# Kernel optimization log

Measured on AMD Instinct MI355X. Metric: run time of the kernel, lower is better.

## Reference

```python
import jax, jax.numpy as jnp
import numpy as np


def _grid_sample_paste(m, boxes, img_h, img_w):
    """Bilinear, align_corners=False, zero padding; separable because the
    affine grid is an outer product of per-row and per-col coordinates.
    m: [N, Hm, Wm] float, boxes: [N, 4] xyxy in output-image coords.
    Returns [N, img_h, img_w]."""
    N, Hm, Wm = m.shape
    x0, y0, x1, y1 = boxes[:, 0:1], boxes[:, 1:2], boxes[:, 2:3], boxes[:, 3:4]
    ys = jnp.arange(img_h, dtype=m.dtype) + 0.5  # pixel centers
    xs = jnp.arange(img_w, dtype=m.dtype) + 0.5
    gy = (ys[None, :] - y0) / (y1 - y0) * 2 - 1  # [N, img_h] in [-1,1]
    gx = (xs[None, :] - x0) / (x1 - x0) * 2 - 1  # [N, img_w]
    # align_corners=False: pixel coord = (g+1)*size/2 - 0.5
    py = (gy + 1) * (Hm * 0.5) - 0.5
    px = (gx + 1) * (Wm * 0.5) - 0.5

    def interp(vals, p, axis, size):
        f = jnp.floor(p)
        i0 = f.astype(jnp.int32)
        w1 = (p - f).astype(vals.dtype)
        w0 = 1.0 - w1

        def gather(idx):
            valid = ((idx >= 0) & (idx < size)).astype(vals.dtype)
            idxc = jnp.clip(idx, 0, size - 1)
            if axis == 2:
                g = jnp.take_along_axis(vals, idxc[:, None, :], axis=2)
                return g * valid[:, None, :]
            else:
                g = jnp.take_along_axis(vals, idxc[:, :, None], axis=1)
                return g * valid[:, :, None]

        if axis == 2:
            return gather(i0) * w0[:, None, :] + gather(i0 + 1) * w1[:, None, :]
        else:
            return gather(i0) * w0[:, :, None] + gather(i0 + 1) * w1[:, :, None]

    mx = interp(m, px, axis=2, size=Wm)   # [N, Hm, img_w]
    return interp(mx, py, axis=1, size=Hm)  # [N, img_h, img_w]


def setup_inputs() -> dict:
    key = jax.random.key(0)
    k1, k2, k3, k4, k5 = jax.random.split(key, 5)
    N, Hm, Wm = 128, 28, 28
    in_h, in_w = 736, 1184
    img_h, img_w = 800, 1280
    masks = jax.random.uniform(k1, (N, 1, Hm, Wm), dtype=jnp.float32)
    # valid xyxy boxes in detector-input coordinates
    bx0 = jax.random.uniform(k2, (N,), minval=0.0, maxval=in_w - 64.0)
    by0 = jax.random.uniform(k3, (N,), minval=0.0, maxval=in_h - 64.0)
    bw = 16.0 + jax.random.uniform(k4, (N,), maxval=256.0)
    bh = 16.0 + jax.random.uniform(k5, (N,), maxval=256.0)
    boxes = jnp.stack([bx0, by0,
                       jnp.minimum(bx0 + bw, in_w * 1.0),
                       jnp.minimum(by0 + bh, in_h * 1.0)], axis=1).astype(jnp.float32)
    return {"masks": masks, "boxes": boxes, "img_h": img_h, "img_w": img_w,
            "in_h": in_h, "in_w": in_w}


def reference(masks, boxes, img_h, img_w, in_h, in_w):
    # my_detector_postprocess: scale boxes to output resolution, clip to image
    sx = img_w / in_w
    sy = img_h / in_h
    scale = jnp.array([sx, sy, sx, sy], dtype=boxes.dtype)
    b = boxes * scale
    b = jnp.stack([jnp.clip(b[:, 0], 0.0, img_w), jnp.clip(b[:, 1], 0.0, img_h),
                   jnp.clip(b[:, 2], 0.0, img_w), jnp.clip(b[:, 3], 0.0, img_h)], axis=1)
    # my_paste_masks_in_image (GPU path, skip_empty=False), soft masks returned
    return _grid_sample_paste(masks[:, 0], b, img_h, img_w)
```

## Files before the change

kernel.cpp:

```cpp
#include <hip/hip_runtime.h>
#include <math.h>

__global__ __launch_bounds__(256) void zero_out(float4* __restrict__ out4, int nf4,
                                                float* __restrict__ out, int out_size) {
    int gid = blockIdx.x * blockDim.x + threadIdx.x;
    int stride = gridDim.x * blockDim.x;
    const float4 z = make_float4(0.f, 0.f, 0.f, 0.f);
    for (int i = gid; i < nf4; i += stride) out4[i] = z;
    if (gid == 0) {
        for (int k = nf4 * 4; k < out_size; ++k) out[k] = 0.f;
    }
}

__device__ __forceinline__ float bilin(const float* __restrict__ r0,
                                       const float* __restrict__ r1,
                                       float px, float vy0, float vy1, int Wm) {
    float fx = floorf(px);
    int ix = (int)fx;
    float wx1 = px - fx;
    float wx0 = 1.f - wx1;
    float vx0 = (ix >= 0 && ix < Wm) ? wx0 : 0.f;
    float vx1 = (ix + 1 >= 0 && ix + 1 < Wm) ? wx1 : 0.f;
    int rx0 = min(max(ix, 0), Wm - 1);
    int rx1 = min(max(ix + 1, 0), Wm - 1);
    float top = r0[rx0] * vx0 + r0[rx1] * vx1;
    float bot = r1[rx0] * vx0 + r1[rx1] * vx1;
    return top * vy0 + bot * vy1;
}

__global__ __launch_bounds__(128) void paint_box(const float* __restrict__ masks,
                       const float* __restrict__ boxes,
                       const int* __restrict__ p_img_h,
                       const int* __restrict__ p_img_w,
                       const int* __restrict__ p_in_h,
                       const int* __restrict__ p_in_w,
                       float* __restrict__ out,
                       int HW, int Hm, int Wm) {
    const int n = blockIdx.x;
    const int img_w = p_img_w[0];
    const int img_h = HW / img_w;

    float fw = (float)img_w, fh = (float)img_h;
    float sx = fw / (float)p_in_w[0];
    float sy = fh / (float)p_in_h[0];
    float x0 = fminf(fmaxf(boxes[4*n+0] * sx, 0.f), fw);
    float y0 = fminf(fmaxf(boxes[4*n+1] * sy, 0.f), fh);
    float x1 = fminf(fmaxf(boxes[4*n+2] * sx, 0.f), fw);
    float y1 = fminf(fmaxf(boxes[4*n+3] * sy, 0.f), fh);
    float swx = (float)Wm / (x1 - x0);
    float swy = (float)Hm / (y1 - y0);

    int xlo = max(0,     (int)floorf(x0 - 0.5f / swx - 0.5f) - 1);
    int xhi = min(img_w, (int)ceilf (x0 + ((float)Wm + 0.5f) / swx - 0.5f) + 2);
    int ylo = max(0,     (int)floorf(y0 - 0.5f / swy - 0.5f) - 1);
    int yhi = min(img_h, (int)ceilf (y0 + ((float)Hm + 0.5f) / swy - 0.5f) + 2);

    const float* mb = masks + (size_t)n * Hm * Wm;
    float* ob = out + (size_t)n * HW;

    for (int y = ylo + blockIdx.y; y < yhi; y += gridDim.y) {
        float py = ((float)y + 0.5f - y0) * swy - 0.5f;
        float fy = floorf(py);
        int iy = (int)fy;
        float wy1 = py - fy, wy0 = 1.f - wy1;
        float vy0 = (iy >= 0 && iy < Hm) ? wy0 : 0.f;
        float vy1 = (iy + 1 >= 0 && iy + 1 < Hm) ? wy1 : 0.f;
        const float* r0 = mb + (size_t)min(max(iy, 0), Hm - 1) * Wm;
        const float* r1 = mb + (size_t)min(max(iy + 1, 0), Hm - 1) * Wm;
        float* orow = ob + (size_t)y * img_w;
        for (int x = xlo + (int)threadIdx.x; x < xhi; x += (int)blockDim.x) {
            float px = ((float)x + 0.5f - x0) * swx - 0.5f;
            orow[x] = bilin(r0, r1, px, vy0, vy1, Wm);
        }
    }
}

extern "C" void kernel_launch(void* const* d_in, const int* in_sizes, int n_in,
                              void* d_out, int out_size, void* d_ws, size_t ws_size,
                              hipStream_t stream) {
    const float* masks  = (const float*)d_in[0];
    const float* boxes  = (const float*)d_in[1];
    const int* p_img_h  = (const int*)d_in[2];
    const int* p_img_w  = (const int*)d_in[3];
    const int* p_in_h   = (const int*)d_in[4];
    const int* p_in_w   = (const int*)d_in[5];

    int N = in_sizes[1] / 4;
    int mask_hw = in_sizes[0] / N;
    int Wm = (int)(sqrtf((float)mask_hw) + 0.5f);
    int Hm = mask_hw / Wm;
    int HW = out_size / N;

    int nf4 = out_size / 4;
    int zblocks = 4096;
    hipLaunchKernelGGL(zero_out, dim3(zblocks), dim3(256), 0, stream,
                       (float4*)d_out, nf4, (float*)d_out, out_size);

    hipLaunchKernelGGL(paint_box, dim3(N, 512), dim3(128), 0, stream,
                       masks, boxes, p_img_h, p_img_w, p_in_h, p_in_w,
                       (float*)d_out, HW, Hm, Wm);
}
```

Measured before the change: 553.9 us.

## Fuse zero-fill and box painting into a single full-image row kernel

Drops the separate zero-fill pass. A new single kernel writes every output pixel once: one block per image row per mask, and each thread produces a float4 of four pixels, storing zeros outside the box. Per-box parameters are precomputed by a tiny setup kernel into workspace. This removes the double write to the box region and the poor occupancy of the old per-box loop, at the cost of an extra small launch and a generic slow fallback path for other image widths.

New measurement: 523.8 us. 5.4% less time.

```diff
diff --git a/kernel.cpp b/kernel.cpp
--- a/kernel.cpp
+++ b/kernel.cpp
@@ -1,20 +1,28 @@
 #include <hip/hip_runtime.h>
 #include <math.h>
 
-__global__ __launch_bounds__(256) void zero_out(float4* __restrict__ out4, int nf4,
-                                                float* __restrict__ out, int out_size) {
-    int gid = blockIdx.x * blockDim.x + threadIdx.x;
-    int stride = gridDim.x * blockDim.x;
-    const float4 z = make_float4(0.f, 0.f, 0.f, 0.f);
-    for (int i = gid; i < nf4; i += stride) out4[i] = z;
-    if (gid == 0) {
-        for (int k = nf4 * 4; k < out_size; ++k) out[k] = 0.f;
-    }
+#define ROWTPB 320
+
+__global__ __launch_bounds__(128) void setup_params(
+        const float* __restrict__ boxes,
+        const int* __restrict__ p_img_h, const int* __restrict__ p_img_w,
+        const int* __restrict__ p_in_h,  const int* __restrict__ p_in_w,
+        float4* __restrict__ params, int N, int Hm, int Wm) {
+    int n = blockIdx.x * blockDim.x + threadIdx.x;
+    if (n >= N) return;
+    float fw = (float)p_img_w[0], fh = (float)p_img_h[0];
+    float sx = fw / (float)p_in_w[0];
+    float sy = fh / (float)p_in_h[0];
+    float x0 = fminf(fmaxf(boxes[4*n+0] * sx, 0.f), fw);
+    float y0 = fminf(fmaxf(boxes[4*n+1] * sy, 0.f), fh);
+    float x1 = fminf(fmaxf(boxes[4*n+2] * sx, 0.f), fw);
+    float y1 = fminf(fmaxf(boxes[4*n+3] * sy, 0.f), fh);
+    params[n] = make_float4(x0, y0, (float)Wm / (x1 - x0), (float)Hm / (y1 - y0));
 }
 
-__device__ __forceinline__ float bilin(const float* __restrict__ r0,
-                                       const float* __restrict__ r1,
-                                       float px, float vy0, float vy1, int Wm) {
+__device__ __forceinline__ float bilinx(const float* __restrict__ r0,
+                                        const float* __restrict__ r1,
+                                        float px, float vy0, float vy1, int Wm) {
     float fx = floorf(px);
     int ix = (int)fx;
     float wx1 = px - fx;
@@ -23,54 +31,77 @@
     float vx1 = (ix + 1 >= 0 && ix + 1 < Wm) ? wx1 : 0.f;
     int rx0 = min(max(ix, 0), Wm - 1);
     int rx1 = min(max(ix + 1, 0), Wm - 1);
-    float top = r0[rx0] * vx0 + r0[rx1] * vx1;
-    float bot = r1[rx0] * vx0 + r1[rx1] * vx1;
-    return top * vy0 + bot * vy1;
+    return (r0[rx0] * vx0 + r0[rx1] * vx1) * vy0
+         + (r1[rx0] * vx0 + r1[rx1] * vx1) * vy1;
 }
 
-__global__ __launch_bounds__(128) void paint_box(const float* __restrict__ masks,
-                       const float* __restrict__ boxes,
-                       const int* __restrict__ p_img_h,
-                       const int* __restrict__ p_img_w,
-                       const int* __restrict__ p_in_h,
-                       const int* __restrict__ p_in_w,
-                       float* __restrict__ out,
-                       int HW, int Hm, int Wm) {
-    const int n = blockIdx.x;
+__device__ __forceinline__ float sample_one(const float* __restrict__ mb,
+                                            float px, float py, int Hm, int Wm) {
+    if (py <= -1.f || py >= (float)Hm || px <= -1.f || px >= (float)Wm) return 0.f;
+    float fy = floorf(py);
+    int iy = (int)fy;
+    float wy1 = py - fy, wy0 = 1.f - wy1;
+    float vy0 = (iy >= 0) ? wy0 : 0.f;
+    float vy1 = (iy + 1 < Hm) ? wy1 : 0.f;
+    const float* r0 = mb + (size_t)max(iy, 0) * Wm;
+    const float* r1 = mb + (size_t)min(iy + 1, Hm - 1) * Wm;
+    return bilinx(r0, r1, px, vy0, vy1, Wm);
+}
+
+__global__ __launch_bounds__(ROWTPB) void paste_rows(
+        const float* __restrict__ masks,
+        const float4* __restrict__ params,
+        const int* __restrict__ p_img_w,
+        float* __restrict__ out,
+        int HW, int Hm, int Wm) {
     const int img_w = p_img_w[0];
-    const int img_h = HW / img_w;
-
-    float fw = (float)img_w, fh = (float)img_h;
-    float sx = fw / (float)p_in_w[0];
-    float sy = fh / (float)p_in_h[0];
-    float x0 = fminf(fmaxf(boxes[4*n+0] * sx, 0.f), fw);
-    float y0 = fminf(fmaxf(boxes[4*n+1] * sy, 0.f), fh);
-    float x1 = fminf(fmaxf(boxes[4*n+2] * sx, 0.f), fw);
-    float y1 = fminf(fmaxf(boxes[4*n+3] * sy, 0.f), fh);
-    float swx = (float)Wm / (x1 - x0);
-    float swy = (float)Hm / (y1 - y0);
-
-    int xlo = max(0,     (int)floorf(x0 - 0.5f / swx - 0.5f) - 1);
-    int xhi = min(img_w, (int)ceilf (x0 + ((float)Wm + 0.5f) / swx - 0.5f) + 2);
-    int ylo = max(0,     (int)floorf(y0 - 0.5f / swy - 0.5f) - 1);
-    int yhi = min(img_h, (int)ceilf (y0 + ((float)Hm + 0.5f) / swy - 0.5f) + 2);
-
+    const int n = blockIdx.y;
+    const float4 P = params[n];
     const float* mb = masks + (size_t)n * Hm * Wm;
     float* ob = out + (size_t)n * HW;
 
-    for (int y = ylo + blockIdx.y; y < yhi; y += gridDim.y) {
-        float py = ((float)y + 0.5f - y0) * swy - 0.5f;
+    if (img_w == ROWTPB * 4) {
+        const int y = blockIdx.x;
+        const int x = (int)threadIdx.x * 4;
+        float* op = ob + (size_t)y * img_w + x;
+
+        float py = ((float)y + 0.5f - P.y) * P.w - 0.5f;
+        if (py <= -1.f || py >= (float)Hm) {
+            *(float4*)op = make_float4(0.f, 0.f, 0.f, 0.f);
+            return;
+        }
         float fy = floorf(py);
         int iy = (int)fy;
         float wy1 = py - fy, wy0 = 1.f - wy1;
-        float vy0 = (iy >= 0 && iy < Hm) ? wy0 : 0.f;
-        float vy1 = (iy + 1 >= 0 && iy + 1 < Hm) ? wy1 : 0.f;
-        const float* r0 = mb + (size_t)min(max(iy, 0), Hm - 1) * Wm;
-        const float* r1 = mb + (size_t)min(max(iy + 1, 0), Hm - 1) * Wm;
-        float* orow = ob + (size_t)y * img_w;
-        for (int x = xlo + (int)threadIdx.x; x < xhi; x += (int)blockDim.x) {
-            float px = ((float)x + 0.5f - x0) * swx - 0.5f;
-            orow[x] = bilin(r0, r1, px, vy0, vy1, Wm);
+        float vy0 = (iy >= 0) ? wy0 : 0.f;
+        float vy1 = (iy + 1 < Hm) ? wy1 : 0.f;
+        const float* r0 = mb + (size_t)max(iy, 0) * Wm;
+        const float* r1 = mb + (size_t)min(iy + 1, Hm - 1) * Wm;
+
+        float px0 = ((float)x + 0.5f - P.x) * P.z - 0.5f;
+        float px3 = px0 + 3.f * P.z;
+        if (px3 <= -1.f || px0 >= (float)Wm) {
+            *(float4*)op = make_float4(0.f, 0.f, 0.f, 0.f);
+            return;
+        }
+        float4 r;
+        r.x = bilinx(r0, r1, px0,            vy0, vy1, Wm);
+        r.y = bilinx(r0, r1, px0 +      P.z, vy0, vy1, Wm);
+        r.z = bilinx(r0, r1, px0 + 2.f* P.z, vy0, vy1, Wm);
+        r.w = bilinx(r0, r1, px3,            vy0, vy1, Wm);
+        *(float4*)op = r;
+    } else {
+        int tid = blockIdx.x * ROWTPB + threadIdx.x;
+        int nthreads = gridDim.x * ROWTPB;
+        for (int base = tid * 4; base < HW; base += nthreads * 4) {
+            for (int i = 0; i < 4 && base + i < HW; ++i) {
+                int idx = base + i;
+                int y = idx / img_w;
+                int x = idx - y * img_w;
+                float py = ((float)y + 0.5f - P.y) * P.w - 0.5f;
+                float px = ((float)x + 0.5f - P.x) * P.z - 0.5f;
+                ob[idx] = sample_one(mb, px, py, Hm, Wm);
+            }
         }
     }
 }
@@ -91,12 +122,14 @@
     int Hm = mask_hw / Wm;
     int HW = out_size / N;
 
-    int nf4 = out_size / 4;
-    int zblocks = 4096;
-    hipLaunchKernelGGL(zero_out, dim3(zblocks), dim3(256), 0, stream,
-                       (float4*)d_out, nf4, (float*)d_out, out_size);
+    float4* params = (float4*)d_ws;
 
-    hipLaunchKernelGGL(paint_box, dim3(N, 512), dim3(128), 0, stream,
-                       masks, boxes, p_img_h, p_img_w, p_in_h, p_in_w,
-                       (float*)d_out, HW, Hm, Wm);
+    hipLaunchKernelGGL(setup_params, dim3((N + 127) / 128), dim3(128), 0, stream,
+                       boxes, p_img_h, p_img_w, p_in_h, p_in_w, params, N, Hm, Wm);
+
+    int rows = HW / (ROWTPB * 4);
+    if (rows < 1) rows = 1;
+    dim3 grid(rows, N);
+    hipLaunchKernelGGL(paste_rows, grid, dim3(ROWTPB), 0, stream,
+                       masks, params, p_img_w, (float*)d_out, HW, Hm, Wm);
 }
```
